# Performance work log

Measured on AMD Instinct MI355X. Metric: run time of the kernel, lower is better.

## Reference

```python
import jax, jax.numpy as jnp
import numpy as np

EMB = 1024
HEADS = 16
S = EMB // HEADS  # 64
B, T = 2, 2048


def setup_inputs() -> dict:
    key = jax.random.key(0)
    ks = jax.random.split(key, 5)
    x = jax.random.normal(ks[0], (B, T, EMB), dtype=jnp.float32)
    Wk = jax.random.normal(ks[1], (S, S), dtype=jnp.float32) * (1.0 / np.sqrt(S))
    Wq = jax.random.normal(ks[2], (S, S), dtype=jnp.float32) * (1.0 / np.sqrt(S))
    Wv = jax.random.normal(ks[3], (S, S), dtype=jnp.float32) * (1.0 / np.sqrt(S))
    Wu = jax.random.normal(ks[4], (EMB, EMB), dtype=jnp.float32) * (1.0 / np.sqrt(EMB))
    bu = jnp.zeros((EMB,), dtype=jnp.float32)
    return {"x": x, "Wk": Wk, "Wq": Wq, "Wv": Wv, "Wu": Wu, "bu": bu}


def reference(x, Wk, Wq, Wv, Wu, bu):
    b, t, e = x.shape
    h, s = HEADS, e // HEADS
    xh = x.reshape(b, t, h, s)
    # torch Linear: y = x @ W.T (per-head projection, weights shared across heads)
    keys = jnp.einsum('bths,os->btho', xh, Wk)
    queries = jnp.einsum('bths,os->btho', xh, Wq)
    values = jnp.einsum('bths,os->btho', xh, Wv)
    scale = e ** (-0.25)
    queries = queries * scale
    keys = keys * scale
    # [b, h, t_q, t_k] full score matrix (as in the original bmm)
    dot = jnp.einsum('bqhd,bkhd->bhqk', queries, keys)
    attn = jax.nn.softmax(dot, axis=-1)
    out = jnp.einsum('bhqk,bkhd->bqhd', attn, values).reshape(b, t, e)
    return out @ Wu.T + bu
```

## Files before the change

### kernel.cpp

```cpp
#include <hip/hip_runtime.h>
#include <hip/hip_bf16.h>
#include <stdint.h>

#define TT   2048
#define EMB  1024
#define SDIM 64
#define KVB  128
#define NIT  (TT / KVB)
#define LOG2E 1.4426950408889634f

typedef float f32x4  __attribute__((ext_vector_type(4)));
typedef float f32x16 __attribute__((ext_vector_type(16)));
typedef short short8 __attribute__((ext_vector_type(8)));
typedef unsigned short ushort4v __attribute__((ext_vector_type(4)));
typedef unsigned int uint2v __attribute__((ext_vector_type(2)));
typedef unsigned int uint4v __attribute__((ext_vector_type(4)));

__device__ __forceinline__ ushort f2bf(float f) {
    uint32_t u = __builtin_bit_cast(uint32_t, f);
    u += 0x7FFFu + ((u >> 16) & 1u);
    return (ushort)(u >> 16);
}

__device__ __forceinline__ short8 cvt8(const float* p) {
    f32x4 a = *(const f32x4*)p;
    f32x4 b = *(const f32x4*)(p + 4);
    short8 r;
    r[0] = (short)f2bf(a[0]); r[1] = (short)f2bf(a[1]);
    r[2] = (short)f2bf(a[2]); r[3] = (short)f2bf(a[3]);
    r[4] = (short)f2bf(b[0]); r[5] = (short)f2bf(b[1]);
    r[6] = (short)f2bf(b[2]); r[7] = (short)f2bf(b[3]);
    return r;
}

__device__ __forceinline__ void gload16(const void* g, void* l) {
    __builtin_amdgcn_global_load_lds((const __attribute__((address_space(1))) uint32_t*)g,
                                     (__attribute__((address_space(3))) uint32_t*)l, 16, 0, 0);
}
__device__ __forceinline__ uint pkbf(float a, float b) {
    uint d; asm("v_cvt_pk_bf16_f32 %0, %1, %2" : "=v"(d) : "v"(a), "v"(b)); return d;
}
__device__ __forceinline__ void swap32(uint& a, uint& b) {
    asm volatile("s_nop 1\n\tv_permlane32_swap_b32 %0, %1" : "+v"(a), "+v"(b));
}
__device__ __forceinline__ float xhadd(float x) {
    uint a = __builtin_bit_cast(uint, x), o;
    asm volatile("v_mov_b32 %0, %1\n\ts_nop 3\n\tv_permlane32_swap_b32 %0, %1"
                 : "=&v"(o), "+v"(a));
    return __builtin_bit_cast(float, o) + __builtin_bit_cast(float, a);
}

__global__ __launch_bounds__(256) void cvt_w(const float* __restrict__ Wk, const float* __restrict__ Wq,
                                             const float* __restrict__ Wv, const float* __restrict__ Wu,
                                             ushort* __restrict__ Wk16, ushort* __restrict__ Wq16,
                                             ushort* __restrict__ Wv16, ushort* __restrict__ Wu16) {
    int i = blockIdx.x * 256 + threadIdx.x;
    Wu16[i] = f2bf(Wu[i]);
    if (i < 4096) {
        Wk16[i] = f2bf(Wk[i]);
        Wq16[i] = f2bf(Wq[i] * (0.03125f * LOG2E));
        Wv16[i] = f2bf(Wv[i]);
    }
}

__global__ __launch_bounds__(256) void qkv(const float* __restrict__ x,
                                           const ushort* __restrict__ Wk16, const ushort* __restrict__ Wq16,
                                           const ushort* __restrict__ Wv16,
                                           ushort* __restrict__ Qw, ushort* __restrict__ Kw, ushort* __restrict__ Vt) {
    const int tid = threadIdx.x;
    const int wave = tid >> 6, lane = tid & 63;
    const int c = lane & 15, g = lane >> 4;
    const int rblk = (blockIdx.x * 4 + wave) * 16;
    const int bh = rblk >> 11;
    const int tbase = rblk & (TT - 1);
    const int b = bh >> 4, h = bh & 15;

    const float* xrow = x + ((size_t)(b * TT + tbase + c) * EMB + h * SDIM);
    short8 a[2];
#pragma unroll
    for (int ks = 0; ks < 2; ++ks) a[ks] = cvt8(xrow + 32 * ks + 8 * g);

    f32x4 aq[4], ak[4], av[4];
#pragma unroll
    for (int n = 0; n < 4; ++n) { aq[n] = 0.f; ak[n] = 0.f; av[n] = 0.f; }

#pragma unroll
    for (int n = 0; n < 4; ++n) {
#pragma unroll
        for (int ks = 0; ks < 2; ++ks) {
            const size_t wo = (size_t)(16 * n + c) * SDIM + 32 * ks + 8 * g;
            short8 bq = *(const short8*)(Wq16 + wo);
            short8 bk = *(const short8*)(Wk16 + wo);
            short8 bv = *(const short8*)(Wv16 + wo);
            aq[n] = __builtin_amdgcn_mfma_f32_16x16x32_bf16(a[ks], bq, aq[n], 0, 0, 0);
            ak[n] = __builtin_amdgcn_mfma_f32_16x16x32_bf16(a[ks], bk, ak[n], 0, 0, 0);
            av[n] = __builtin_amdgcn_mfma_f32_16x16x32_bf16(a[ks], bv, av[n], 0, 0, 0);
        }
    }
    const size_t hb = (size_t)bh * TT * SDIM;
#pragma unroll
    for (int n = 0; n < 4; ++n) {
#pragma unroll
        for (int i = 0; i < 4; ++i) {
            const size_t o = hb + (size_t)(tbase + 4 * g + i) * SDIM + 16 * n + c;
            Qw[o] = f2bf(aq[n][i]);
            Kw[o] = f2bf(ak[n][i]);
        }
        ushort4v vp;
#pragma unroll
        for (int i = 0; i < 4; ++i) vp[i] = f2bf(av[n][i]);
        *(ushort4v*)(Vt + hb + (size_t)(16 * n + c) * TT + tbase + 4 * g) = vp;
    }
}

__global__ __launch_bounds__(256) void attn(const ushort* __restrict__ Qw, const ushort* __restrict__ Kw,
                                            const ushort* __restrict__ Vt, ushort* __restrict__ AO) {
    __shared__ ushort smem[4][8192];

    const int tid = threadIdx.x;
    const int wv = tid >> 6, lane = tid & 63;
    const int q = lane & 31, hi = lane >> 5;

    const int wg = blockIdx.x;
    const int xcd = wg & 7, slot = wg >> 3;
    const int bh = xcd * 4 + (slot >> 4);
    const int qt = slot & 15;
    const int b = bh >> 4, h = bh & 15;
    const int qrowW = qt * 128 + wv * 32;
    const size_t base = (size_t)bh * TT * SDIM;

    short8 qa[4];
    const ushort* Qp = Qw + base + (size_t)(qrowW + q) * SDIM + 8 * hi;
#pragma unroll
    for (int sb = 0; sb < 4; ++sb) qa[sb] = *(const short8*)(Qp + 16 * sb);

    f32x16 a0v = 0.f, a1v = 0.f;
    float lsum = 0.f;

    const int krow = lane >> 3;
    const ushort* Ks = Kw + base + (size_t)(wv * 8 + krow) * SDIM + (((lane & 7) ^ krow) * 8);
    const int vrow = wv * 4 + (lane >> 4);
    const ushort* Vs = Vt + base + (size_t)vrow * TT + (((lane & 15) ^ (vrow & 15)) * 8);

#define STAGE(kvb, buf) { \
    char* kb = (char*)&smem[(buf)][0] + wv * 1024;      \
    char* vb = (char*)&smem[2 + (buf)][0] + wv * 1024;  \
    _Pragma("unroll")                                    \
    for (int p = 0; p < 4; ++p) {                        \
        gload16(Ks + (kvb) * 64 + p * 2048, kb + p * 4096); \
        gload16(Vs + (kvb) + p * 16 * TT,   vb + p * 4096); \
    } }

    STAGE(0, 0);
    __syncthreads();

    const int kmask = (q & 7) << 4;
    const int vmask = q & 15;
    int cur = 0;
    for (int kt = 0; kt < NIT; ++kt) {
        if (kt < NIT - 1) STAGE((kt + 1) * KVB, cur ^ 1);
        const char* Kc = (const char*)&smem[cur][0];
        const char* Vc = (const char*)&smem[2 + cur][0];

        f32x16 s0 = 0.f, s1 = 0.f, s2 = 0.f, s3 = 0.f;
#pragma unroll
        for (int sb = 0; sb < 4; ++sb) {
            const int off = (32 * sb + 16 * hi) ^ kmask;
            short8 k0 = *(const short8*)(Kc + q * 128 + off);
            s0 = __builtin_amdgcn_mfma_f32_32x32x16_bf16(k0, qa[sb], s0, 0, 0, 0);
            short8 k1 = *(const short8*)(Kc + (32 + q) * 128 + off);
            s1 = __builtin_amdgcn_mfma_f32_32x32x16_bf16(k1, qa[sb], s1, 0, 0, 0);
            short8 k2 = *(const short8*)(Kc + (64 + q) * 128 + off);
            s2 = __builtin_amdgcn_mfma_f32_32x32x16_bf16(k2, qa[sb], s2, 0, 0, 0);
            short8 k3 = *(const short8*)(Kc + (96 + q) * 128 + off);
            s3 = __builtin_amdgcn_mfma_f32_32x32x16_bf16(k3, qa[sb], s3, 0, 0, 0);
        }

        float r0 = 0.f, r1 = 0.f, r2 = 0.f, r3 = 0.f;
#pragma unroll
        for (int i = 0; i < 16; ++i) { float p = __builtin_amdgcn_exp2f(s0[i]); s0[i] = p; r0 += p; }
#pragma unroll
        for (int i = 0; i < 16; ++i) { float p = __builtin_amdgcn_exp2f(s1[i]); s1[i] = p; r1 += p; }
#pragma unroll
        for (int i = 0; i < 16; ++i) { float p = __builtin_amdgcn_exp2f(s2[i]); s2[i] = p; r2 += p; }
#pragma unroll
        for (int i = 0; i < 16; ++i) { float p = __builtin_amdgcn_exp2f(s3[i]); s3[i] = p; r3 += p; }
        lsum += (r0 + r1) + (r2 + r3);

        short8 pb0, pb1, pb2, pb3, pb4, pb5, pb6, pb7;
#define RP(sv, pa_, pb_) { \
        uint u0 = pkbf(sv[0], sv[1]),   u1 = pkbf(sv[2], sv[3]);   \
        uint u2 = pkbf(sv[4], sv[5]),   u3 = pkbf(sv[6], sv[7]);   \
        swap32(u0, u2); swap32(u1, u3);                            \
        uint4v ta = {u0, u1, u2, u3}; pa_ = __builtin_bit_cast(short8, ta); \
        uint u4 = pkbf(sv[8], sv[9]),   u5 = pkbf(sv[10], sv[11]); \
        uint u6 = pkbf(sv[12], sv[13]), u7 = pkbf(sv[14], sv[15]); \
        swap32(u4, u6); swap32(u5, u7);                            \
        uint4v tb = {u4, u5, u6, u7}; pb_ = __builtin_bit_cast(short8, tb); }
        RP(s0, pb0, pb1) RP(s1, pb2, pb3) RP(s2, pb4, pb5) RP(s3, pb6, pb7)
#undef RP

#define PV(kstep, pbk) { \
        const int u = ((2 * (kstep) + hi) ^ vmask) << 4;                   \
        short8 v0 = *(const short8*)(Vc + q * 256 + u);                    \
        a0v = __builtin_amdgcn_mfma_f32_32x32x16_bf16(v0, pbk, a0v, 0, 0, 0); \
        short8 v1 = *(const short8*)(Vc + (32 + q) * 256 + u);             \
        a1v = __builtin_amdgcn_mfma_f32_32x32x16_bf16(v1, pbk, a1v, 0, 0, 0); }
        PV(0, pb0) PV(1, pb1) PV(2, pb2) PV(3, pb3)
        PV(4, pb4) PV(5, pb5) PV(6, pb6) PV(7, pb7)
#undef PV

        __syncthreads();
        cur ^= 1;
    }
#undef STAGE

    const float l_i = xhadd(lsum);
    char* scrB = (char*)(&smem[0][0] + wv * 2048);
    const int eswz = (q & 7) << 4;
    float inv = 1.f / l_i;
#pragma unroll
    for (int sb2 = 0; sb2 < 2; ++sb2) {
#pragma unroll
        for (int bq = 0; bq < 4; ++bq) {
            float v0 = (sb2 ? a1v[4 * bq + 0] : a0v[4 * bq + 0]) * inv;
            float v1 = (sb2 ? a1v[4 * bq + 1] : a0v[4 * bq + 1]) * inv;
            float v2 = (sb2 ? a1v[4 * bq + 2] : a0v[4 * bq + 2]) * inv;
            float v3 = (sb2 ? a1v[4 * bq + 3] : a0v[4 * bq + 3]) * inv;
            uint2v d; d[0] = pkbf(v0, v1); d[1] = pkbf(v2, v3);
            int s0e = 8 * bq + 4 * hi + 32 * sb2;
            *(uint2v*)(scrB + q * 128 + ((s0e * 2) ^ eswz)) = d;
        }
    }
    asm volatile("s_waitcnt lgkmcnt(0)" ::: "memory");
    ushort* AOp = AO + (size_t)(b * TT + qrowW + q) * EMB + h * SDIM + 32 * hi;
#pragma unroll
    for (int jj = 0; jj < 4; ++jj) {
        short8 o = *(const short8*)(scrB + q * 128 + ((64 * hi + 16 * jj) ^ eswz));
        *(short8*)(AOp + 8 * jj) = o;
    }
}

__global__ __launch_bounds__(512) void oproj(const ushort* __restrict__ AO, const ushort* __restrict__ Wu16,
                                             const float* __restrict__ bu, float* __restrict__ out) {
    __shared__ ushort Ab[2][128 * 64];
    __shared__ ushort Bb[2][128 * 64];
    const int tid = threadIdx.x;
    const int wv = tid >> 6, lane = tid & 63;
    const int c = lane & 15, g = lane >> 4;
    const int wr = wv >> 1, wc = wv & 1;
    const int rblk = blockIdx.x * 128, nblk = blockIdx.y * 128;

    const int row0 = tid >> 3;
    const int col0 = ((tid & 7) ^ (row0 & 7)) * 8;
    const ushort* As0 = AO   + (size_t)(rblk + row0) * EMB + col0;
    const ushort* As1 = AO   + (size_t)(rblk + row0 + 64) * EMB + col0;
    const ushort* Bs0 = Wu16 + (size_t)(nblk + row0) * EMB + col0;
    const ushort* Bs1 = Wu16 + (size_t)(nblk + row0 + 64) * EMB + col0;
    const int l0 = wv * 512, l1 = 4096 + wv * 512;

    f32x4 acc[2][4];
#pragma unroll
    for (int m = 0; m < 2; ++m)
#pragma unroll
        for (int n = 0; n < 4; ++n) acc[m][n] = 0.f;

    gload16(As0, &Ab[0][l0]); gload16(As1, &Ab[0][l1]);
    gload16(Bs0, &Bb[0][l0]); gload16(Bs1, &Bb[0][l1]);
    __syncthreads();

    const int swzA = (c & 7) << 4;
    int cur = 0;
    for (int kt = 0; kt < 16; ++kt) {
        if (kt < 15) {
            const int k0 = (kt + 1) * 64;
            gload16(As0 + k0, &Ab[cur ^ 1][l0]); gload16(As1 + k0, &Ab[cur ^ 1][l1]);
            gload16(Bs0 + k0, &Bb[cur ^ 1][l0]); gload16(Bs1 + k0, &Bb[cur ^ 1][l1]);
        }
        const char* Ac = (const char*)&Ab[cur][0];
        const char* Bc = (const char*)&Bb[cur][0];
#pragma unroll
        for (int kb = 0; kb < 2; ++kb) {
            short8 am[2], bn[4];
#pragma unroll
            for (int m = 0; m < 2; ++m)
                am[m] = *(const short8*)(Ac + (wr * 32 + 16 * m + c) * 128 + ((64 * kb + 16 * g) ^ swzA));
#pragma unroll
            for (int n = 0; n < 4; ++n)
                bn[n] = *(const short8*)(Bc + (wc * 64 + 16 * n + c) * 128 + ((64 * kb + 16 * g) ^ swzA));
#pragma unroll
            for (int m = 0; m < 2; ++m)
#pragma unroll
                for (int n = 0; n < 4; ++n)
                    acc[m][n] = __builtin_amdgcn_mfma_f32_16x16x32_bf16(am[m], bn[n], acc[m][n], 0, 0, 0);
        }
        __syncthreads();
        cur ^= 1;
    }
#pragma unroll
    for (int m = 0; m < 2; ++m)
#pragma unroll
        for (int n = 0; n < 4; ++n) {
            float bias = bu[nblk + wc * 64 + 16 * n + c];
#pragma unroll
            for (int i = 0; i < 4; ++i)
                out[(size_t)(rblk + wr * 32 + 16 * m + 4 * g + i) * EMB + nblk + wc * 64 + 16 * n + c] =
                    acc[m][n][i] + bias;
        }
}

extern "C" void kernel_launch(void* const* d_in, const int* in_sizes, int n_in,
                              void* d_out, int out_size, void* d_ws, size_t ws_size,
                              hipStream_t stream) {
    const float* x  = (const float*)d_in[0];
    const float* Wk = (const float*)d_in[1];
    const float* Wq = (const float*)d_in[2];
    const float* Wv = (const float*)d_in[3];
    const float* Wu = (const float*)d_in[4];
    const float* bu = (const float*)d_in[5];
    float* out = (float*)d_out;

    char* ws = (char*)d_ws;
    const size_t MB = 1024u * 1024u;
    ushort* Qw   = (ushort*)(ws);
    ushort* Kw   = (ushort*)(ws + 8 * MB);
    ushort* Vt   = (ushort*)(ws + 16 * MB);
    ushort* AO   = (ushort*)(ws + 24 * MB);
    ushort* Wu16 = (ushort*)(ws + 32 * MB);
    ushort* Wk16 = (ushort*)(ws + 34 * MB);
    ushort* Wq16 = Wk16 + 4096;
    ushort* Wv16 = Wk16 + 8192;

    cvt_w<<<dim3(4096), dim3(256), 0, stream>>>(Wk, Wq, Wv, Wu, Wk16, Wq16, Wv16, Wu16);
    qkv<<<dim3(1024), dim3(256), 0, stream>>>(x, Wk16, Wq16, Wv16, Qw, Kw, Vt);
    attn<<<dim3(512), dim3(256), 0, stream>>>(Qw, Kw, Vt, AO);
    oproj<<<dim3(32, 8), dim3(512), 0, stream>>>(AO, Wu16, bu, out);
}
```

Measured before the change: 88.84 us.

## Split each KV tile across two wave groups in attention and reduce partials

The attention block grows from 4 to 8 waves. Each group of four waves handles half of every 128-key tile: it computes 64 scores per query row and does half of the PV accumulation. At the end, the second group writes its partial output accumulators and row sums to shared memory, and the first group adds them before normalising and storing. The aim is more waves per CU and a shorter serial chain of MFMA and exp work per wave. The cost is an extra cross-wave reduction through LDS, one more barrier, and each wave doing fewer loads in the staging loop.

```diff
diff --git a/kernel.cpp b/kernel.cpp
--- a/kernel.cpp
+++ b/kernel.cpp
@@ -9,6 +9,7 @@
 #define NIT  (TT / KVB)
 #define LOG2E 1.4426950408889634f
 
+typedef float f32x2  __attribute__((ext_vector_type(2)));
 typedef float f32x4  __attribute__((ext_vector_type(4)));
 typedef float f32x16 __attribute__((ext_vector_type(16)));
 typedef short short8 __attribute__((ext_vector_type(8)));
@@ -113,20 +114,22 @@
     }
 }
 
-__global__ __launch_bounds__(256) void attn(const ushort* __restrict__ Qw, const ushort* __restrict__ Kw,
-                                            const ushort* __restrict__ Vt, ushort* __restrict__ AO) {
+__global__ __launch_bounds__(512, 4) void attn(const ushort* __restrict__ Qw, const ushort* __restrict__ Kw,
+                                               const ushort* __restrict__ Vt, ushort* __restrict__ AO) {
     __shared__ ushort smem[4][8192];
 
     const int tid = threadIdx.x;
     const int wv = tid >> 6, lane = tid & 63;
     const int q = lane & 31, hi = lane >> 5;
+    const int qg = wv & 3, kh = wv >> 2;
+    const int wo = kh * 64;
 
     const int wg = blockIdx.x;
     const int xcd = wg & 7, slot = wg >> 3;
     const int bh = xcd * 4 + (slot >> 4);
     const int qt = slot & 15;
     const int b = bh >> 4, h = bh & 15;
-    const int qrowW = qt * 128 + wv * 32;
+    const int qrowW = qt * 128 + qg * 32;
     const size_t base = (size_t)bh * TT * SDIM;
 
     short8 qa[4];
@@ -146,9 +149,9 @@
     char* kb = (char*)&smem[(buf)][0] + wv * 1024;      \
     char* vb = (char*)&smem[2 + (buf)][0] + wv * 1024;  \
     _Pragma("unroll")                                    \
-    for (int p = 0; p < 4; ++p) {                        \
-        gload16(Ks + (kvb) * 64 + p * 2048, kb + p * 4096); \
-        gload16(Vs + (kvb) + p * 16 * TT,   vb + p * 4096); \
+    for (int p = 0; p < 2; ++p) {                        \
+        gload16(Ks + (kvb) * 64 + p * 4096, kb + p * 8192); \
+        gload16(Vs + (kvb) + p * 32 * TT,   vb + p * 8192); \
     } }
 
     STAGE(0, 0);
@@ -162,32 +165,24 @@
         const char* Kc = (const char*)&smem[cur][0];
         const char* Vc = (const char*)&smem[2 + cur][0];
 
-        f32x16 s0 = 0.f, s1 = 0.f, s2 = 0.f, s3 = 0.f;
+        f32x16 s0 = 0.f, s1 = 0.f;
 #pragma unroll
         for (int sb = 0; sb < 4; ++sb) {
             const int off = (32 * sb + 16 * hi) ^ kmask;
-            short8 k0 = *(const short8*)(Kc + q * 128 + off);
+            short8 k0 = *(const short8*)(Kc + (wo + q) * 128 + off);
             s0 = __builtin_amdgcn_mfma_f32_32x32x16_bf16(k0, qa[sb], s0, 0, 0, 0);
-            short8 k1 = *(const short8*)(Kc + (32 + q) * 128 + off);
+            short8 k1 = *(const short8*)(Kc + (wo + 32 + q) * 128 + off);
             s1 = __builtin_amdgcn_mfma_f32_32x32x16_bf16(k1, qa[sb], s1, 0, 0, 0);
-            short8 k2 = *(const short8*)(Kc + (64 + q) * 128 + off);
-            s2 = __builtin_amdgcn_mfma_f32_32x32x16_bf16(k2, qa[sb], s2, 0, 0, 0);
-            short8 k3 = *(const short8*)(Kc + (96 + q) * 128 + off);
-            s3 = __builtin_amdgcn_mfma_f32_32x32x16_bf16(k3, qa[sb], s3, 0, 0, 0);
-        }
-
-        float r0 = 0.f, r1 = 0.f, r2 = 0.f, r3 = 0.f;
+        }
+
+        float r0 = 0.f, r1 = 0.f;
 #pragma unroll
         for (int i = 0; i < 16; ++i) { float p = __builtin_amdgcn_exp2f(s0[i]); s0[i] = p; r0 += p; }
 #pragma unroll
         for (int i = 0; i < 16; ++i) { float p = __builtin_amdgcn_exp2f(s1[i]); s1[i] = p; r1 += p; }
-#pragma unroll
-        for (int i = 0; i < 16; ++i) { float p = __builtin_amdgcn_exp2f(s2[i]); s2[i] = p; r2 += p; }
-#pragma unroll
-        for (int i = 0; i < 16; ++i) { float p = __builtin_amdgcn_exp2f(s3[i]); s3[i] = p; r3 += p; }
-        lsum += (r0 + r1) + (r2 + r3);
-
-        short8 pb0, pb1, pb2, pb3, pb4, pb5, pb6, pb7;
+        lsum += r0 + r1;
+
+        short8 pb0, pb1, pb2, pb3;
 #define RP(sv, pa_, pb_) { \
         uint u0 = pkbf(sv[0], sv[1]),   u1 = pkbf(sv[2], sv[3]);   \
         uint u2 = pkbf(sv[4], sv[5]),   u3 = pkbf(sv[6], sv[7]);   \
@@ -197,17 +192,16 @@
         uint u6 = pkbf(sv[12], sv[13]), u7 = pkbf(sv[14], sv[15]); \
         swap32(u4, u6); swap32(u5, u7);                            \
         uint4v tb = {u4, u5, u6, u7}; pb_ = __builtin_bit_cast(short8, tb); }
-        RP(s0, pb0, pb1) RP(s1, pb2, pb3) RP(s2, pb4, pb5) RP(s3, pb6, pb7)
+        RP(s0, pb0, pb1) RP(s1, pb2, pb3)
 #undef RP
 
 #define PV(kstep, pbk) { \
-        const int u = ((2 * (kstep) + hi) ^ vmask) << 4;                   \
+        const int u = ((2 * (kstep) + hi + kh * 8) ^ vmask) << 4;          \
         short8 v0 = *(const short8*)(Vc + q * 256 + u);                    \
         a0v = __builtin_amdgcn_mfma_f32_32x32x16_bf16(v0, pbk, a0v, 0, 0, 0); \
         short8 v1 = *(const short8*)(Vc + (32 + q) * 256 + u);             \
         a1v = __builtin_amdgcn_mfma_f32_32x32x16_bf16(v1, pbk, a1v, 0, 0, 0); }
         PV(0, pb0) PV(1, pb1) PV(2, pb2) PV(3, pb3)
-        PV(4, pb4) PV(5, pb5) PV(6, pb6) PV(7, pb7)
 #undef PV
 
         __syncthreads();
@@ -215,8 +209,27 @@
     }
 #undef STAGE
 
+    f32x2* ob = (f32x2*)&smem[0][0];
+    float* lb = (float*)&smem[0][0] + 8192;
+    const int mb = qg * 1024 + lane;
+    if (kh) {
+#pragma unroll
+        for (int j = 0; j < 8; ++j) { f32x2 t = {a0v[2 * j], a0v[2 * j + 1]}; ob[mb + j * 64] = t; }
+#pragma unroll
+        for (int j = 0; j < 8; ++j) { f32x2 t = {a1v[2 * j], a1v[2 * j + 1]}; ob[mb + (8 + j) * 64] = t; }
+        lb[qg * 64 + lane] = lsum;
+    }
+    __syncthreads();
+    if (kh) return;
+
+#pragma unroll
+    for (int j = 0; j < 8; ++j) { f32x2 t = ob[mb + j * 64];       a0v[2 * j] += t[0]; a0v[2 * j + 1] += t[1]; }
+#pragma unroll
+    for (int j = 0; j < 8; ++j) { f32x2 t = ob[mb + (8 + j) * 64]; a1v[2 * j] += t[0]; a1v[2 * j + 1] += t[1]; }
+    lsum += lb[qg * 64 + lane];
+
     const float l_i = xhadd(lsum);
-    char* scrB = (char*)(&smem[0][0] + wv * 2048);
+    char* scrB = (char*)&smem[0][0] + 40960 + qg * 4096;
     const int eswz = (q & 7) << 4;
     float inv = 1.f / l_i;
 #pragma unroll
@@ -333,6 +346,6 @@
 
     cvt_w<<<dim3(4096), dim3(256), 0, stream>>>(Wk, Wq, Wv, Wu, Wk16, Wq16, Wv16, Wu16);
     qkv<<<dim3(1024), dim3(256), 0, stream>>>(x, Wk16, Wq16, Wv16, Qw, Kw, Vt);
-    attn<<<dim3(512), dim3(256), 0, stream>>>(Qw, Kw, Vt, AO);
+    attn<<<dim3(512), dim3(512), 0, stream>>>(Qw, Kw, Vt, AO);
     oproj<<<dim3(32, 8), dim3(512), 0, stream>>>(AO, Wu16, bu, out);
 }
```

New measurement: 84.58 us. 4.8% less time.
